# Kernel optimization log

Hardware: AMD Instinct MI355X
Metric: run time of the kernel (lower is better)

The kernel has to match this reference:

```python
import jax, jax.numpy as jnp
import numpy as np

TOPK = 4
ROUTE_SCALE = 1.0


def setup_inputs() -> dict:
    key = jax.random.key(0)
    ks = jax.random.split(key, 16)
    B, S, C, D = 4, 512, 4, 2048
    E, H = 16, 1408
    SH = 2 * H  # n_shared_experts * moe_inter_dim
    s = 0.02
    return {
        "embeddings": jax.random.normal(ks[0], (B, S, C, D), jnp.float32),
        "x": jax.random.normal(ks[1], (B, S, C, 1), jnp.float32),
        "Wg": jax.random.normal(ks[2], (E, D), jnp.float32) * s,
        "W1": jax.random.normal(ks[3], (E, H, D), jnp.float32) * s,
        "b1": jax.random.normal(ks[4], (E, H), jnp.float32) * s,
        "W2": jax.random.normal(ks[5], (E, D, H), jnp.float32) * s,
        "b2": jax.random.normal(ks[6], (E, D), jnp.float32) * s,
        "W3": jax.random.normal(ks[7], (E, H, D), jnp.float32) * s,
        "b3": jax.random.normal(ks[8], (E, H), jnp.float32) * s,
        "Ws1": jax.random.normal(ks[9], (SH, D), jnp.float32) * s,
        "bs1": jax.random.normal(ks[10], (SH,), jnp.float32) * s,
        "Ws2": jax.random.normal(ks[11], (D, SH), jnp.float32) * s,
        "bs2": jax.random.normal(ks[12], (D,), jnp.float32) * s,
    }


def reference(embeddings, x, Wg, W1, b1, W2, b2, W3, b3, Ws1, bs1, Ws2, bs2):
    # NOTE: in the torch module, the `x` arg is immediately shadowed by
    # embeddings.view(-1, dim); it does not participate in the math.
    D = Wg.shape[1]
    E = Wg.shape[0]
    xt = embeddings.reshape(-1, D)  # [N, D] flattened tokens

    # Gate: softmax scores (fp32), top-k routing; n_groups == 1, no gate bias.
    logits = jnp.einsum("nd,ed->ne", xt, Wg)
    scores = jax.nn.softmax(logits.astype(jnp.float32), axis=-1)  # [N, E]
    topv, idx = jax.lax.top_k(scores, TOPK)  # values == gathered original scores
    weights = (topv * ROUTE_SCALE).astype(xt.dtype)  # [N, K]

    # Expert dispatch/combine. Per-token combined weight for expert e is
    # sum_k weights[n, k] * (idx[n, k] == e); unassigned tokens get weight 0,
    # so masked-dense per-expert SwiGLU reproduces the gather/scatter math.
    y = jnp.zeros_like(xt)
    for e in range(E):
        w_e = jnp.sum(weights * (idx == e).astype(weights.dtype), axis=1)  # [N]
        h = jax.nn.silu(xt @ W1[e].T + b1[e]) * (xt @ W3[e].T + b3[e])  # [N, H]
        y = y + (h @ W2[e].T + b2[e]) * w_e[:, None]

    # Shared experts: Linear -> SiLU -> Linear applied to every token.
    z = jax.nn.silu(xt @ Ws1.T + bs1) @ Ws2.T + bs2

    return (y + z).reshape(embeddings.shape)
```

## Files before the change

kernel.cpp:

```cpp
#include <hip/hip_runtime.h>
#include <stdint.h>

#define N_TOK 8192
#define DIM   2048
#define NEXP  16
#define HID   1408
#define SHID  2816
#define KTOP  4
#define TILEMAX 272

typedef __attribute__((ext_vector_type(8))) short bf16x8;
typedef __attribute__((ext_vector_type(4))) float f32x4;

#define MFMA16(a,b,c) __builtin_amdgcn_mfma_f32_16x16x32_bf16((a),(b),(c),0,0,0)

#define WAIT_ALL()  asm volatile("s_waitcnt vmcnt(0) lgkmcnt(0)" ::: "memory")
#define BARRIER()   asm volatile("s_barrier" ::: "memory")

__device__ __forceinline__ unsigned short f2b(float f){
  unsigned u = __float_as_uint(f);
  return (unsigned short)((u + 0x7fffu + ((u >> 16) & 1u)) >> 16);
}
__device__ __forceinline__ unsigned pk2(float a, float b){
  return (unsigned)f2b(a) | ((unsigned)f2b(b) << 16);
}
__device__ __forceinline__ float bu2f(unsigned hs){ return __uint_as_float(hs << 16); }
__device__ __forceinline__ float siluf(float x){ return x / (1.f + expf(-x)); }
__device__ __forceinline__ f32x4 zero4(){ f32x4 z; z[0]=0.f; z[1]=0.f; z[2]=0.f; z[3]=0.f; return z; }

__device__ __forceinline__ void gll16(const unsigned short* g, unsigned short* l){
  __builtin_amdgcn_global_load_lds(
      (const __attribute__((address_space(1))) void*)g,
      (__attribute__((address_space(3))) void*)l, 16, 0, 0);
}

#define SEGW ((size_t)NEXP*HID*DIM/4)
#define SEGS ((size_t)SHID*DIM/4)
__global__ __launch_bounds__(256) void k_cvtW(const float* __restrict__ W1, const float* __restrict__ W3,
                                              const float* __restrict__ W2, const float* __restrict__ Ws1,
                                              const float* __restrict__ Ws2,
                                              unsigned short* __restrict__ d1, unsigned short* __restrict__ d3,
                                              unsigned short* __restrict__ d2, unsigned short* __restrict__ ds1,
                                              unsigned short* __restrict__ ds2){
  size_t total = 3*SEGW + 2*SEGS;
  for (size_t i = (size_t)blockIdx.x*256 + threadIdx.x; i < total; i += (size_t)gridDim.x*256){
    const float* s; unsigned short* d; size_t off;
    if      (i <   SEGW)        { s = W1;  d = d1;  off = i; }
    else if (i < 2*SEGW)        { s = W3;  d = d3;  off = i - SEGW; }
    else if (i < 3*SEGW)        { s = W2;  d = d2;  off = i - 2*SEGW; }
    else if (i < 3*SEGW + SEGS) { s = Ws1; d = ds1; off = i - 3*SEGW; }
    else                        { s = Ws2; d = ds2; off = i - 3*SEGW - SEGS; }
    float4 v = ((const float4*)s)[off];
    uint2 q; q.x = pk2(v.x, v.y); q.y = pk2(v.z, v.w);
    ((uint2*)d)[off] = q;
  }
}

__global__ __launch_bounds__(256) void k_gate(const float* __restrict__ X, const float* __restrict__ Wg,
                                              float* __restrict__ topw, int* __restrict__ topi,
                                              int* __restrict__ cnt, unsigned short* __restrict__ Xb){
  int lane = threadIdx.x & 63;
  int t = blockIdx.x*4 + (threadIdx.x >> 6);
  const float* xr = X + (size_t)t*DIM;
  float4 xv[8];
#pragma unroll
  for (int i=0;i<8;i++){
    xv[i] = *(const float4*)(xr + i*256 + lane*4);
    uint2 q; q.x = pk2(xv[i].x, xv[i].y); q.y = pk2(xv[i].z, xv[i].w);
    *(uint2*)(Xb + (size_t)t*DIM + i*256 + lane*4) = q;
  }
  float sc[NEXP];
#pragma unroll
  for (int e=0;e<NEXP;e++){
    const float* wr = Wg + e*DIM;
    float s = 0.f;
#pragma unroll
    for (int i=0;i<8;i++){
      float4 w = *(const float4*)(wr + i*256 + lane*4);
      s = fmaf(xv[i].x, w.x, s); s = fmaf(xv[i].y, w.y, s);
      s = fmaf(xv[i].z, w.z, s); s = fmaf(xv[i].w, w.w, s);
    }
#pragma unroll
    for (int d=1; d<64; d<<=1) s += __shfl_xor(s, d);
    sc[e] = s;
  }
  if (lane == 0){
    float m = sc[0];
#pragma unroll
    for (int e=1;e<NEXP;e++) m = fmaxf(m, sc[e]);
    float den = 0.f;
#pragma unroll
    for (int e=0;e<NEXP;e++){ sc[e] = expf(sc[e]-m); den += sc[e]; }
    float inv = 1.f/den;
#pragma unroll
    for (int e=0;e<NEXP;e++) sc[e] *= inv;
    for (int k=0;k<KTOP;k++){
      int bi = 0; float bv = sc[0];
#pragma unroll
      for (int e=1;e<NEXP;e++) if (sc[e] > bv){ bv = sc[e]; bi = e; }
      topw[t*KTOP+k] = bv;
      topi[t*KTOP+k] = bi;
#pragma unroll
      for (int e=0;e<NEXP;e++) if (e == bi) sc[e] = -1.f;
      atomicAdd(&cnt[bi], 1);
    }
  }
}

__global__ void k_scan(const int* __restrict__ cnt, int* __restrict__ off, int* __restrict__ cur,
                       int* __restrict__ tab){
  if (threadIdx.x == 0){
    int a = 0;
    for (int e=0;e<NEXP;e++){ off[e] = a; cur[e] = a; a += cnt[e]; }
    int n = 0;
    for (int e=0;e<NEXP;e++){
      int nt = (cnt[e] + 127) >> 7;
      for (int r=0;r<nt;r++) tab[n++] = (e << 16) | r;
    }
    for (; n < TILEMAX; ++n) tab[n] = -1;
  }
}

__global__ __launch_bounds__(256) void k_place(const int* __restrict__ topi, const float* __restrict__ topw,
                                               int* __restrict__ cur, int* __restrict__ rows,
                                               float* __restrict__ rw, int* __restrict__ slotL){
  int t = blockIdx.x*256 + threadIdx.x;
#pragma unroll
  for (int k=0;k<KTOP;k++){
    int e = topi[t*KTOP+k];
    int p = atomicAdd(&cur[e], 1);
    rows[p] = t;
    rw[p]   = topw[t*KTOP+k];
    slotL[t*KTOP+k] = p;
  }
}

__device__ __forceinline__ void stage_Bf(unsigned short* lsB, const float* bF,
                                         int ldK, int bn0, int k0, int tid){
#pragma unroll
  for (int j=0;j<8;j++){
    int idx = j*256 + tid, r = idx >> 4, c4 = idx & 15;
    float4 v = *(const float4*)(bF + (size_t)(bn0 + r)*ldK + k0 + c4*4);
    uint2 q; q.x = pk2(v.x, v.y); q.y = pk2(v.z, v.w);
    *(uint2*)&lsB[r*64 + (((c4 >> 1) ^ (r & 7)) << 3) + ((c4 & 1) << 2)] = q;
  }
}

__device__ __forceinline__ void stage_Bf32(unsigned short* lsB, const float* bF,
                                           int bn0, int k0, int tid){
#pragma unroll
  for (int j=0;j<4;j++){
    int idx = j*256 + tid;
    int r = idx >> 3, c4 = idx & 7;
    float4 v = *(const float4*)(bF + (size_t)(bn0 + r)*DIM + k0 + c4*4);
    uint2 q; q.x = pk2(v.x, v.y); q.y = pk2(v.z, v.w);
    *(uint2*)&lsB[r*32 + (((c4 >> 1) ^ ((r >> 1) & 3)) << 3) + ((c4 & 1) << 2)] = q;
  }
}

__device__ __forceinline__ void read_A(bf16x8 af[4], const unsigned short* lsA, int wm, int lane, int kc){
  int s = kc*4 + (lane >> 4);
#pragma unroll
  for (int mi=0;mi<4;mi++){
    int r = wm + mi*16 + (lane & 15);
    af[mi] = *(const bf16x8*)&lsA[r*64 + ((s ^ (r & 7)) << 3)];
  }
}

__device__ __forceinline__ void read_A32(bf16x8 af[4], const unsigned short* lsA, int wm, int lane){
  int s = lane >> 4;
#pragma unroll
  for (int mi=0;mi<4;mi++){
    int r = wm + mi*16 + (lane & 15);
    af[mi] = *(const bf16x8*)&lsA[r*32 + ((s ^ ((r >> 1) & 3)) << 3)];
  }
}

template<bool WBF>
__global__ __launch_bounds__(256,2) void k_g13(const unsigned short* __restrict__ Xb,
    const void* __restrict__ W1p, const void* __restrict__ W3p,
    const float* __restrict__ b1, const float* __restrict__ b3,
    const int* __restrict__ rows, const int* __restrict__ cnt, const int* __restrict__ offs,
    const int* __restrict__ tab, unsigned short* __restrict__ H1)
{
  int bid = blockIdx.x;
  int l = bid >> 3;
  int ct = l / 34;
  int slot = (bid & 7)*34 + (l - ct*34);
  int ent = tab[slot];
  if (ent < 0) return;
  int e = ent >> 16, rt = ent & 0xffff;
  int cntE = cnt[e];
  int offE = offs[e];
  int hn0 = ct*128;
  int tid = threadIdx.x, lane = tid & 63, wid = tid >> 6;
  int wm = (wid >> 1)*64, wn = (wid & 1)*64;
  __shared__ alignas(16) unsigned short lsA[2][4096], lsB1[2][4096], lsB3[2][4096];

  int r0 = tid >> 2;
  int sl = tid & 3;
  int cxg = sl ^ ((r0 >> 1) & 3);
  unsigned offA[2];
#pragma unroll
  for (int j=0;j<2;j++){
    int lrow = rt*128 + r0 + j*64;
    int arow = rows[offE + (lrow < cntE ? lrow : cntE-1)];
    offA[j] = (unsigned)arow*DIM + (unsigned)cxg*8;
  }
  unsigned offB0 = (unsigned)(hn0 + r0)*DIM + (unsigned)cxg*8;
  const unsigned short* b1H = (const unsigned short*)W1p + (size_t)e*HID*DIM;
  const unsigned short* b3H = (const unsigned short*)W3p + (size_t)e*HID*DIM;
  const float* b1F = (const float*)W1p + (size_t)e*HID*DIM;
  const float* b3F = (const float*)W3p + (size_t)e*HID*DIM;
  unsigned dst0 = (unsigned)tid*8;

  f32x4 acc1[4][4], acc3[4][4];
#pragma unroll
  for (int i=0;i<4;i++)
#pragma unroll
    for (int j=0;j<4;j++){ acc1[i][j] = zero4(); acc3[i][j] = zero4(); }

  auto STAGE = [&](int set, int k0){
#pragma unroll
    for (int j=0;j<2;j++){
      gll16(Xb + offA[j] + k0, &lsA[set][dst0 + j*2048]);
      if constexpr (WBF){
        gll16(b1H + offB0 + j*(64*DIM) + k0, &lsB1[set][dst0 + j*2048]);
        gll16(b3H + offB0 + j*(64*DIM) + k0, &lsB3[set][dst0 + j*2048]);
      }
    }
    if constexpr (!WBF){
      stage_Bf32(lsB1[set], b1F, hn0, k0, tid);
      stage_Bf32(lsB3[set], b3F, hn0, k0, tid);
    }
  };

  STAGE(0, 0);
  WAIT_ALL();
  BARRIER();
  int cur = 0;
  for (int kt=0; kt<DIM/32; ++kt){
    if (kt+1 < DIM/32) STAGE(cur^1, (kt+1)*32);
    bf16x8 af[4]; read_A32(af, lsA[cur], wm, lane);
    int s = lane >> 4;
#pragma unroll
    for (int nj=0;nj<4;nj++){
      int rb = wn + nj*16 + (lane & 15);
      int lof = rb*32 + ((s ^ ((rb >> 1) & 3)) << 3);
      bf16x8 bf1 = *(const bf16x8*)&lsB1[cur][lof];
      bf16x8 bf3 = *(const bf16x8*)&lsB3[cur][lof];
#pragma unroll
      for (int mi=0;mi<4;mi++){
        acc1[mi][nj] = MFMA16(af[mi], bf1, acc1[mi][nj]);
        acc3[mi][nj] = MFMA16(af[mi], bf3, acc3[mi][nj]);
      }
    }
    WAIT_ALL();
    BARRIER();
    cur ^= 1;
  }
#pragma unroll
  for (int nj=0;nj<4;nj++){
    int h = hn0 + wn + nj*16 + (lane & 15);
    float b1v = b1[e*HID + h];
    float b3v = b3[e*HID + h];
#pragma unroll
    for (int mi=0;mi<4;mi++){
#pragma unroll
      for (int r=0;r<4;r++){
        int gr = rt*128 + wm + mi*16 + (lane >> 4)*4 + r;
        if (gr < cntE){
          float u = acc1[mi][nj][r] + b1v;
          float v = acc3[mi][nj][r] + b3v;
          H1[(size_t)(offE + gr)*HID + h] = f2b(siluf(u)*v);
        }
      }
    }
  }
}

template<int MODE, bool WBF, int KSTEPS>
__global__ __launch_bounds__(256,2) void k_gemm(const unsigned short* __restrict__ Abase,
    const void* __restrict__ Bpv, const float* __restrict__ bias,
    float* __restrict__ outF, unsigned short* __restrict__ outH,
    const int* __restrict__ rows, const float* __restrict__ rw,
    const int* __restrict__ cnt, const int* __restrict__ offs,
    const int* __restrict__ tab)
{
  constexpr int KD = KSTEPS*64;
  int e = 0, ct, rt, cntE = 0, offE = 0;
  int bid = blockIdx.x;
  int l = bid >> 3;
  if constexpr (MODE >= 2){
    ct = l / 34;
    int slot = (bid & 7)*34 + (l - ct*34);
    int ent = tab[slot];
    if (ent < 0) return;
    e = ent >> 16; rt = ent & 0xffff;
    cntE = cnt[e];
    offE = offs[e];
  } else {
    rt = (bid & 7)*8 + (l & 7);
    ct = l >> 3;
  }
  int bn0 = ct*128, t0 = rt*128;
  int tid = threadIdx.x, lane = tid & 63, wid = tid >> 6;
  int wm = (wid >> 1)*64, wn = (wid & 1)*64;
  __shared__ alignas(16) unsigned short lsA[2][8192], lsB[2][8192];

  int lr8 = lane >> 3;
  int cx  = (lane & 7) ^ lr8;
  unsigned offA0 = 0;
  unsigned offA[4];
  if constexpr (MODE >= 2){
#pragma unroll
    for (int j=0;j<4;j++){
      int lrow = t0 + wid*32 + j*8 + lr8;
      int arow = offE + (lrow < cntE ? lrow : cntE-1);
      offA[j] = (unsigned)arow*KD + (unsigned)cx*8;
    }
  } else {
    offA0 = (unsigned)(t0 + wid*32 + lr8)*KD + (unsigned)cx*8;
  }
  unsigned offB0 = (unsigned)(bn0 + wid*32 + lr8)*KD + (unsigned)cx*8;
  const unsigned short* bH = (const unsigned short*)Bpv + ((MODE >= 2) ? (size_t)e*2048*KD : (size_t)0);
  const float*          bF = (const float*)Bpv          + ((MODE >= 2) ? (size_t)e*2048*KD : (size_t)0);
  const float* biasp = bias + ((MODE >= 2) ? e*DIM : 0);

  f32x4 acc[4][4];
#pragma unroll
  for (int i=0;i<4;i++)
#pragma unroll
    for (int j=0;j<4;j++) acc[i][j] = zero4();

  auto STAGE = [&](int set, int k0){
#pragma unroll
    for (int j=0;j<4;j++){
      if constexpr (MODE >= 2) gll16(Abase + offA[j] + k0, &lsA[set][wid*2048 + j*512]);
      else                     gll16(Abase + offA0 + j*(8*KD) + k0, &lsA[set][wid*2048 + j*512]);
      if constexpr (WBF)       gll16(bH + offB0 + j*(8*KD) + k0, &lsB[set][wid*2048 + j*512]);
    }
    if constexpr (!WBF) stage_Bf(lsB[set], bF, KD, bn0, k0, tid);
  };

  STAGE(0, 0);
  WAIT_ALL();
  BARRIER();
  int cur = 0;
  for (int kt=0; kt<KSTEPS; ++kt){
    if (kt+1 < KSTEPS) STAGE(cur^1, (kt+1)*64);
#pragma unroll
    for (int kc=0;kc<2;kc++){
      bf16x8 af[4]; read_A(af, lsA[cur], wm, lane, kc);
      int sB = kc*4 + (lane >> 4);
#pragma unroll
      for (int nj=0;nj<4;nj++){
        int rb = wn + nj*16 + (lane & 15);
        bf16x8 bfr = *(const bf16x8*)&lsB[cur][rb*64 + ((sB ^ (rb & 7)) << 3)];
#pragma unroll
        for (int mi=0;mi<4;mi++)
          acc[mi][nj] = MFMA16(af[mi], bfr, acc[mi][nj]);
      }
    }
    WAIT_ALL();
    BARRIER();
    cur ^= 1;
  }
#pragma unroll
  for (int nj=0;nj<4;nj++){
    int col = bn0 + wn + nj*16 + (lane & 15);
    float bv = biasp[col];
#pragma unroll
    for (int mi=0;mi<4;mi++){
#pragma unroll
      for (int r=0;r<4;r++){
        int lr = wm + mi*16 + (lane >> 4)*4 + r;
        float v = acc[mi][nj][r] + bv;
        if constexpr (MODE == 0){
          outH[(size_t)(t0 + lr)*SHID + col] = f2b(siluf(v));
        } else if constexpr (MODE == 1){
          outF[(size_t)(t0 + lr)*DIM + col] = v;
        } else {
          int gr = t0 + lr;
          if (gr < cntE){
            int slot = offE + gr;
            float wv = rw[slot] * v;
            if constexpr (MODE == 2){
              atomicAdd(outF + (size_t)rows[slot]*DIM + col, wv);
            } else {
              outH[(size_t)slot*DIM + col] = f2b(wv);
            }
          }
        }
      }
    }
  }
}

__global__ __launch_bounds__(256) void k_comb(const unsigned short* __restrict__ Yr,
                                              const int* __restrict__ slotL, float* __restrict__ out){
  int i = blockIdx.x*256 + threadIdx.x;
  int t = i >> 8, c = i & 255;
  size_t ob = (size_t)t*DIM + (size_t)c*8;
  float4 a = *(float4*)(out + ob);
  float4 b = *(float4*)(out + ob + 4);
  int sl[4];
#pragma unroll
  for (int k=0;k<KTOP;k++) sl[k] = slotL[t*KTOP + k];
#pragma unroll
  for (int k=0;k<KTOP;k++){
    uint4 v = *(const uint4*)(Yr + (size_t)sl[k]*DIM + (size_t)c*8);
    a.x += bu2f(v.x & 0xffffu); a.y += bu2f(v.x >> 16);
    a.z += bu2f(v.y & 0xffffu); a.w += bu2f(v.y >> 16);
    b.x += bu2f(v.z & 0xffffu); b.y += bu2f(v.z >> 16);
    b.z += bu2f(v.w & 0xffffu); b.w += bu2f(v.w >> 16);
  }
  *(float4*)(out + ob) = a;
  *(float4*)(out + ob + 4) = b;
}

extern "C" void kernel_launch(void* const* d_in, const int* in_sizes, int n_in,
                              void* d_out, int out_size, void* d_ws, size_t ws_size,
                              hipStream_t stream)
{
  (void)in_sizes; (void)n_in; (void)out_size;
  const float* emb = (const float*)d_in[0];
  const float* Wg  = (const float*)d_in[2];
  const float* W1  = (const float*)d_in[3];
  const float* b1  = (const float*)d_in[4];
  const float* W2  = (const float*)d_in[5];
  const float* b2  = (const float*)d_in[6];
  const float* W3  = (const float*)d_in[7];
  const float* b3  = (const float*)d_in[8];
  const float* Ws1 = (const float*)d_in[9];
  const float* bs1 = (const float*)d_in[10];
  const float* Ws2 = (const float*)d_in[11];
  const float* bs2 = (const float*)d_in[12];
  float* out = (float*)d_out;
  char* ws = (char*)d_ws;

  const size_t SZ_XB = (size_t)N_TOK*DIM*2;
  const size_t SZ_H1 = (size_t)N_TOK*KTOP*HID*2;
  const size_t SZ_HS = (size_t)N_TOK*SHID*2;
  const size_t SZ_T4 = (size_t)N_TOK*KTOP*4;
  const size_t SZ_WB = (size_t)NEXP*HID*DIM*2;
  const size_t SZ_SB = (size_t)SHID*DIM*2;
  const size_t SZ_YR = (size_t)N_TOK*KTOP*DIM*2;

  size_t off_xb = 0;
  size_t off_h1 = off_xb + SZ_XB;
  size_t off_hs = off_h1 + SZ_H1;
  size_t off_tw = off_hs + SZ_HS;
  size_t off_ti = off_tw + SZ_T4;
  size_t off_ro = off_ti + SZ_T4;
  size_t off_rw = off_ro + SZ_T4;
  size_t off_sl = off_rw + SZ_T4;
  size_t off_cnt = off_sl + SZ_T4;
  size_t off_off = off_cnt + 256;
  size_t off_cur = off_off + 256;
  size_t off_tab = off_cur + 256;
  size_t base_end = off_tab + TILEMAX*4 + 64;
  size_t off_w1b = base_end;
  size_t off_w3b = off_w1b + SZ_WB;
  size_t off_w2b = off_w3b + SZ_WB;
  size_t off_s1b = off_w2b + SZ_WB;
  size_t off_s2b = off_s1b + SZ_SB;
  size_t wbf_end = off_s2b + SZ_SB;

  bool wbf = ws_size >= wbf_end;
  size_t off_yr = wbf ? wbf_end : base_end;
  bool comb = ws_size >= off_yr + SZ_YR;

  unsigned short* Xb = (unsigned short*)(ws + off_xb);
  unsigned short* H1 = (unsigned short*)(ws + off_h1);
  unsigned short* Hs = (unsigned short*)(ws + off_hs);
  float* topw = (float*)(ws + off_tw);
  int*   topi = (int*)(ws + off_ti);
  int*   rowsL= (int*)(ws + off_ro);
  float* rwL  = (float*)(ws + off_rw);
  int*   slotL= (int*)(ws + off_sl);
  int*   cntP = (int*)(ws + off_cnt);
  int*   offP = (int*)(ws + off_off);
  int*   curP = (int*)(ws + off_cur);
  int*   tabP = (int*)(ws + off_tab);
  unsigned short* Yr = (unsigned short*)(ws + off_yr);

  hipMemsetAsync(ws + off_cnt, 0, 768, stream);
  if (wbf){
    k_cvtW<<<4096, 256, 0, stream>>>(W1, W3, W2, Ws1, Ws2,
        (unsigned short*)(ws + off_w1b), (unsigned short*)(ws + off_w3b),
        (unsigned short*)(ws + off_w2b), (unsigned short*)(ws + off_s1b),
        (unsigned short*)(ws + off_s2b));
  }
  k_gate<<<2048, 256, 0, stream>>>(emb, Wg, topw, topi, cntP, Xb);
  k_scan<<<1, 64, 0, stream>>>(cntP, offP, curP, tabP);
  k_place<<<32, 256, 0, stream>>>(topi, topw, curP, rowsL, rwL, slotL);

  if (wbf) k_g13<true ><<<2992, 256, 0, stream>>>(Xb, ws+off_w1b, ws+off_w3b, b1, b3, rowsL, cntP, offP, tabP, H1);
  else     k_g13<false><<<2992, 256, 0, stream>>>(Xb, W1, W3, b1, b3, rowsL, cntP, offP, tabP, H1);

  if (wbf) k_gemm<0,true ,32><<<1408, 256, 0, stream>>>(Xb, ws+off_s1b, bs1, nullptr, Hs, nullptr,nullptr,nullptr,nullptr,nullptr);
  else     k_gemm<0,false,32><<<1408, 256, 0, stream>>>(Xb, Ws1, bs1, nullptr, Hs, nullptr,nullptr,nullptr,nullptr,nullptr);

  if (wbf) k_gemm<1,true ,44><<<1024, 256, 0, stream>>>(Hs, ws+off_s2b, bs2, out, nullptr, nullptr,nullptr,nullptr,nullptr,nullptr);
  else     k_gemm<1,false,44><<<1024, 256, 0, stream>>>(Hs, Ws2, bs2, out, nullptr, nullptr,nullptr,nullptr,nullptr,nullptr);

  if (comb){
    if (wbf) k_gemm<3,true ,22><<<4352, 256, 0, stream>>>(H1, ws+off_w2b, b2, nullptr, Yr, rowsL, rwL, cntP, offP, tabP);
    else     k_gemm<3,false,22><<<4352, 256, 0, stream>>>(H1, W2, b2, nullptr, Yr, rowsL, rwL, cntP, offP, tabP);
    k_comb<<<N_TOK, 256, 0, stream>>>(Yr, slotL, out);
  } else {
    if (wbf) k_gemm<2,true ,22><<<4352, 256, 0, stream>>>(H1, ws+off_w2b, b2, out, nullptr, rowsL, rwL, cntP, offP, tabP);
    else     k_gemm<2,false,22><<<4352, 256, 0, stream>>>(H1, W2, b2, out, nullptr, rowsL, rwL, cntP, offP, tabP);
  }
}
```

Baseline: 2.079 ms.

## Deepen GEMM pipelines to triple/quad LDS buffering with partial vmcnt waits

The expert gate/up kernel moves from double to triple LDS buffering, and the generic GEMM moves from a 64-wide double-buffered K tile to a 32-wide quad-buffered one. Each uses partial s_waitcnt vmcnt waits, so several global_load_lds stages stay in flight while MFMAs run. This is meant to hide global-memory latency better than the old wait-everything-then-barrier pattern. In exchange the K step is smaller, so there are more barriers per tile, LDS use changes, and correctness depends on the vmcnt counts matching the loads issued per stage.

After: 2.166 ms. +4.1%, slower.

```diff
diff --git a/kernel.cpp b/kernel.cpp
--- a/kernel.cpp
+++ b/kernel.cpp
@@ -14,8 +14,11 @@
 
 #define MFMA16(a,b,c) __builtin_amdgcn_mfma_f32_16x16x32_bf16((a),(b),(c),0,0,0)
 
-#define WAIT_ALL()  asm volatile("s_waitcnt vmcnt(0) lgkmcnt(0)" ::: "memory")
-#define BARRIER()   asm volatile("s_barrier" ::: "memory")
+#define WAIT_VM(n)  do { asm volatile("s_waitcnt vmcnt(" #n ") lgkmcnt(0)" ::: "memory"); \
+                         __builtin_amdgcn_sched_barrier(0); } while(0)
+#define WAIT_ALL()  do { asm volatile("s_waitcnt vmcnt(0) lgkmcnt(0)" ::: "memory"); \
+                         __builtin_amdgcn_sched_barrier(0); } while(0)
+#define BARRIER()   __builtin_amdgcn_s_barrier()
 
 __device__ __forceinline__ unsigned short f2b(float f){
   unsigned u = __float_as_uint(f);
@@ -135,17 +138,6 @@
   }
 }
 
-__device__ __forceinline__ void stage_Bf(unsigned short* lsB, const float* bF,
-                                         int ldK, int bn0, int k0, int tid){
-#pragma unroll
-  for (int j=0;j<8;j++){
-    int idx = j*256 + tid, r = idx >> 4, c4 = idx & 15;
-    float4 v = *(const float4*)(bF + (size_t)(bn0 + r)*ldK + k0 + c4*4);
-    uint2 q; q.x = pk2(v.x, v.y); q.y = pk2(v.z, v.w);
-    *(uint2*)&lsB[r*64 + (((c4 >> 1) ^ (r & 7)) << 3) + ((c4 & 1) << 2)] = q;
-  }
-}
-
 __device__ __forceinline__ void stage_Bf32(unsigned short* lsB, const float* bF,
                                            int bn0, int k0, int tid){
 #pragma unroll
@@ -157,13 +149,15 @@
     *(uint2*)&lsB[r*32 + (((c4 >> 1) ^ ((r >> 1) & 3)) << 3) + ((c4 & 1) << 2)] = q;
   }
 }
-
-__device__ __forceinline__ void read_A(bf16x8 af[4], const unsigned short* lsA, int wm, int lane, int kc){
-  int s = kc*4 + (lane >> 4);
-#pragma unroll
-  for (int mi=0;mi<4;mi++){
-    int r = wm + mi*16 + (lane & 15);
-    af[mi] = *(const bf16x8*)&lsA[r*64 + ((s ^ (r & 7)) << 3)];
+__device__ __forceinline__ void stage_Bf32K(unsigned short* lsB, const float* bF,
+                                            int ldK, int bn0, int k0, int tid){
+#pragma unroll
+  for (int j=0;j<4;j++){
+    int idx = j*256 + tid;
+    int r = idx >> 3, c4 = idx & 7;
+    float4 v = *(const float4*)(bF + (size_t)(bn0 + r)*ldK + k0 + c4*4);
+    uint2 q; q.x = pk2(v.x, v.y); q.y = pk2(v.z, v.w);
+    *(uint2*)&lsB[r*32 + (((c4 >> 1) ^ ((r >> 1) & 3)) << 3) + ((c4 & 1) << 2)] = q;
   }
 }
 
@@ -195,7 +189,7 @@
   int hn0 = ct*128;
   int tid = threadIdx.x, lane = tid & 63, wid = tid >> 6;
   int wm = (wid >> 1)*64, wn = (wid & 1)*64;
-  __shared__ alignas(16) unsigned short lsA[2][4096], lsB1[2][4096], lsB3[2][4096];
+  __shared__ alignas(16) unsigned short lsA[3][4096], lsB1[3][4096], lsB3[3][4096];
 
   int r0 = tid >> 2;
   int sl = tid & 3;
@@ -235,12 +229,15 @@
     }
   };
 
+  constexpr int KS = DIM/32;
   STAGE(0, 0);
-  WAIT_ALL();
-  BARRIER();
-  int cur = 0;
-  for (int kt=0; kt<DIM/32; ++kt){
-    if (kt+1 < DIM/32) STAGE(cur^1, (kt+1)*32);
+  STAGE(1, 32);
+  int cur = 0, stg = 2;
+  for (int kt=0; kt<KS; ++kt){
+    if (kt+1 < KS) { if constexpr (WBF) WAIT_VM(6); else WAIT_ALL(); }
+    else           WAIT_ALL();
+    BARRIER();
+    if (kt+2 < KS) STAGE(stg, (kt+2)*32);
     bf16x8 af[4]; read_A32(af, lsA[cur], wm, lane);
     int s = lane >> 4;
 #pragma unroll
@@ -255,9 +252,8 @@
         acc3[mi][nj] = MFMA16(af[mi], bf3, acc3[mi][nj]);
       }
     }
-    WAIT_ALL();
-    BARRIER();
-    cur ^= 1;
+    cur = (cur == 2) ? 0 : cur + 1;
+    stg = (stg == 2) ? 0 : stg + 1;
   }
 #pragma unroll
   for (int nj=0;nj<4;nj++){
@@ -287,7 +283,7 @@
     const int* __restrict__ cnt, const int* __restrict__ offs,
     const int* __restrict__ tab)
 {
-  constexpr int KD = KSTEPS*64;
+  constexpr int KD = KSTEPS*32;
   int e = 0, ct, rt, cntE = 0, offE = 0;
   int bid = blockIdx.x;
   int l = bid >> 3;
@@ -306,26 +302,25 @@
   int bn0 = ct*128, t0 = rt*128;
   int tid = threadIdx.x, lane = tid & 63, wid = tid >> 6;
   int wm = (wid >> 1)*64, wn = (wid & 1)*64;
-  __shared__ alignas(16) unsigned short lsA[2][8192], lsB[2][8192];
-
-  int lr8 = lane >> 3;
-  int cx  = (lane & 7) ^ lr8;
-  unsigned offA0 = 0;
-  unsigned offA[4];
-  if constexpr (MODE >= 2){
-#pragma unroll
-    for (int j=0;j<4;j++){
-      int lrow = t0 + wid*32 + j*8 + lr8;
-      int arow = offE + (lrow < cntE ? lrow : cntE-1);
-      offA[j] = (unsigned)arow*KD + (unsigned)cx*8;
-    }
-  } else {
-    offA0 = (unsigned)(t0 + wid*32 + lr8)*KD + (unsigned)cx*8;
-  }
-  unsigned offB0 = (unsigned)(bn0 + wid*32 + lr8)*KD + (unsigned)cx*8;
+  __shared__ alignas(16) unsigned short lsA[4][4096], lsB[4][4096];
+
+  int r0 = tid >> 2;
+  int sl = tid & 3;
+  int cxg = sl ^ ((r0 >> 1) & 3);
+  unsigned offA[2];
+#pragma unroll
+  for (int j=0;j<2;j++){
+    int lrow = t0 + r0 + j*64;
+    int arow;
+    if constexpr (MODE >= 2) arow = offE + (lrow < cntE ? lrow : cntE-1);
+    else                     arow = lrow;
+    offA[j] = (unsigned)arow*KD + (unsigned)cxg*8;
+  }
+  unsigned offB0 = (unsigned)(bn0 + r0)*KD + (unsigned)cxg*8;
   const unsigned short* bH = (const unsigned short*)Bpv + ((MODE >= 2) ? (size_t)e*2048*KD : (size_t)0);
   const float*          bF = (const float*)Bpv          + ((MODE >= 2) ? (size_t)e*2048*KD : (size_t)0);
   const float* biasp = bias + ((MODE >= 2) ? e*DIM : 0);
+  unsigned dst0 = (unsigned)tid*8;
 
   f32x4 acc[4][4];
 #pragma unroll
@@ -335,36 +330,35 @@
 
   auto STAGE = [&](int set, int k0){
 #pragma unroll
-    for (int j=0;j<4;j++){
-      if constexpr (MODE >= 2) gll16(Abase + offA[j] + k0, &lsA[set][wid*2048 + j*512]);
-      else                     gll16(Abase + offA0 + j*(8*KD) + k0, &lsA[set][wid*2048 + j*512]);
-      if constexpr (WBF)       gll16(bH + offB0 + j*(8*KD) + k0, &lsB[set][wid*2048 + j*512]);
-    }
-    if constexpr (!WBF) stage_Bf(lsB[set], bF, KD, bn0, k0, tid);
+    for (int j=0;j<2;j++){
+      gll16(Abase + offA[j] + k0, &lsA[set][dst0 + j*2048]);
+      if constexpr (WBF) gll16(bH + offB0 + j*(64*KD) + k0, &lsB[set][dst0 + j*2048]);
+    }
+    if constexpr (!WBF) stage_Bf32K(lsB[set], bF, KD, bn0, k0, tid);
   };
 
   STAGE(0, 0);
-  WAIT_ALL();
-  BARRIER();
-  int cur = 0;
+  STAGE(1, 32);
+  STAGE(2, 64);
   for (int kt=0; kt<KSTEPS; ++kt){
-    if (kt+1 < KSTEPS) STAGE(cur^1, (kt+1)*64);
-#pragma unroll
-    for (int kc=0;kc<2;kc++){
-      bf16x8 af[4]; read_A(af, lsA[cur], wm, lane, kc);
-      int sB = kc*4 + (lane >> 4);
-#pragma unroll
-      for (int nj=0;nj<4;nj++){
-        int rb = wn + nj*16 + (lane & 15);
-        bf16x8 bfr = *(const bf16x8*)&lsB[cur][rb*64 + ((sB ^ (rb & 7)) << 3)];
-#pragma unroll
-        for (int mi=0;mi<4;mi++)
-          acc[mi][nj] = MFMA16(af[mi], bfr, acc[mi][nj]);
-      }
-    }
-    WAIT_ALL();
+    if constexpr (WBF){
+      if      (kt+2 < KSTEPS) WAIT_VM(8);
+      else if (kt+1 < KSTEPS) WAIT_VM(4);
+      else                    WAIT_ALL();
+    } else WAIT_ALL();
     BARRIER();
-    cur ^= 1;
+    if (kt+3 < KSTEPS) STAGE((kt+3) & 3, (kt+3)*32);
+    int cur = kt & 3;
+    bf16x8 af[4]; read_A32(af, lsA[cur], wm, lane);
+    int s = lane >> 4;
+#pragma unroll
+    for (int nj=0;nj<4;nj++){
+      int rb = wn + nj*16 + (lane & 15);
+      bf16x8 bfr = *(const bf16x8*)&lsB[cur][rb*32 + ((s ^ ((rb >> 1) & 3)) << 3)];
+#pragma unroll
+      for (int mi=0;mi<4;mi++)
+        acc[mi][nj] = MFMA16(af[mi], bfr, acc[mi][nj]);
+    }
   }
 #pragma unroll
   for (int nj=0;nj<4;nj++){
@@ -499,18 +493,18 @@
   if (wbf) k_g13<true ><<<2992, 256, 0, stream>>>(Xb, ws+off_w1b, ws+off_w3b, b1, b3, rowsL, cntP, offP, tabP, H1);
   else     k_g13<false><<<2992, 256, 0, stream>>>(Xb, W1, W3, b1, b3, rowsL, cntP, offP, tabP, H1);
 
-  if (wbf) k_gemm<0,true ,32><<<1408, 256, 0, stream>>>(Xb, ws+off_s1b, bs1, nullptr, Hs, nullptr,nullptr,nullptr,nullptr,nullptr);
-  else     k_gemm<0,false,32><<<1408, 256, 0, stream>>>(Xb, Ws1, bs1, nullptr, Hs, nullptr,nullptr,nullptr,nullptr,nullptr);
-
-  if (wbf) k_gemm<1,true ,44><<<1024, 256, 0, stream>>>(Hs, ws+off_s2b, bs2, out, nullptr, nullptr,nullptr,nullptr,nullptr,nullptr);
-  else     k_gemm<1,false,44><<<1024, 256, 0, stream>>>(Hs, Ws2, bs2, out, nullptr, nullptr,nullptr,nullptr,nullptr,nullptr);
+  if (wbf) k_gemm<0,true ,64><<<1408, 256, 0, stream>>>(Xb, ws+off_s1b, bs1, nullptr, Hs, nullptr,nullptr,nullptr,nullptr,nullptr);
+  else     k_gemm<0,false,64><<<1408, 256, 0, stream>>>(Xb, Ws1, bs1, nullptr, Hs, nullptr,nullptr,nullptr,nullptr,nullptr);
+
+  if (wbf) k_gemm<1,true ,88><<<1024, 256, 0, stream>>>(Hs, ws+off_s2b, bs2, out, nullptr, nullptr,nullptr,nullptr,nullptr,nullptr);
+  else     k_gemm<1,false,88><<<1024, 256, 0, stream>>>(Hs, Ws2, bs2, out, nullptr, nullptr,nullptr,nullptr,nullptr,nullptr);
 
   if (comb){
-    if (wbf) k_gemm<3,true ,22><<<4352, 256, 0, stream>>>(H1, ws+off_w2b, b2, nullptr, Yr, rowsL, rwL, cntP, offP, tabP);
-    else     k_gemm<3,false,22><<<4352, 256, 0, stream>>>(H1, W2, b2, nullptr, Yr, rowsL, rwL, cntP, offP, tabP);
+    if (wbf) k_gemm<3,true ,44><<<4352, 256, 0, stream>>>(H1, ws+off_w2b, b2, nullptr, Yr, rowsL, rwL, cntP, offP, tabP);
+    else     k_gemm<3,false,44><<<4352, 256, 0, stream>>>(H1, W2, b2, nullptr, Yr, rowsL, rwL, cntP, offP, tabP);
     k_comb<<<N_TOK, 256, 0, stream>>>(Yr, slotL, out);
   } else {
-    if (wbf) k_gemm<2,true ,22><<<4352, 256, 0, stream>>>(H1, ws+off_w2b, b2, out, nullptr, rowsL, rwL, cntP, offP, tabP);
-    else     k_gemm<2,false,22><<<4352, 256, 0, stream>>>(H1, W2, b2, out, nullptr, rowsL, rwL, cntP, offP, tabP);
-  }
-}
+    if (wbf) k_gemm<2,true ,44><<<4352, 256, 0, stream>>>(H1, ws+off_w2b, b2, out, nullptr, rowsL, rwL, cntP, offP, tabP);
+    else     k_gemm<2,false,44><<<4352, 256, 0, stream>>>(H1, W2, b2, out, nullptr, rowsL, rwL, cntP, offP, tabP);
+  }
+}
```
